# Performance work log

Hardware: AMD Instinct MI355X
Metric: run time of the kernel (lower is better)

## Reference

```python
import jax, jax.numpy as jnp
import numpy as np

POOLING_RATIO = 0.5  # matches init kwarg
N_NODES = 16384
N_EDGES = 524288
D_FEAT = 128


def setup_inputs() -> dict:
    key = jax.random.key(0)
    k1, k2, k3, k4 = jax.random.split(key, 4)
    return {
        "pos": jax.random.normal(k1, (N_NODES, 3), jnp.float32),
        "feat": jax.random.normal(k2, (N_NODES, D_FEAT), jnp.float32),
        "src": jax.random.randint(k3, (N_EDGES,), 0, N_NODES, jnp.int32),
        "dst": jax.random.randint(k4, (N_EDGES,), 0, N_NODES, jnp.int32),
        "batch_size": 4,
    }


def _fps(p, k):
    # Farthest point sampling on one cloud p: [n, 3]. Deterministic start at idx 0
    # (DGL uses a random start; we fix it for reproducibility).
    n = p.shape[0]
    def step(carry, _):
        dists, last = carry  # dists: min sq-dist to selected set so far
        d = jnp.sum((p - p[last]) ** 2, axis=-1)
        dists = jnp.minimum(dists, d)
        nxt = jnp.argmax(dists).astype(jnp.int32)
        return (dists, nxt), last
    init = (jnp.full((n,), 1e10, p.dtype), jnp.asarray(0, jnp.int32))
    _, idx = jax.lax.scan(step, init, None, length=k)
    return idx  # [k]


def reference(pos, feat, src, dst, batch_size):
    N = pos.shape[0]
    n_points = N // batch_size
    k = round(n_points * (1.0 - POOLING_RATIO))  # downsampled points per cloud

    # ---- farthest point sampling per cloud ----
    p = pos.reshape(batch_size, n_points, pos.shape[-1])  # [B, n, 3]
    fp = jax.vmap(lambda q: _fps(q, k))(p)                # [B, k] local ids
    offs = (jnp.arange(batch_size, dtype=jnp.int32) * n_points)[:, None]
    fp_idx = (fp + offs).reshape(-1)                      # [B*k] global ids

    # ---- copy_u + mean aggregation on the FULL graph (G.update_all) ----
    deg = jax.ops.segment_sum(jnp.ones_like(dst, dtype=feat.dtype), dst, num_segments=N)
    agg = jax.ops.segment_sum(feat[src], dst, num_segments=N)  # [N, D]
    agg = agg / jnp.maximum(deg, 1.0)[:, None]  # nodes with no in-edges stay 0

    # ---- induced subgraph gather ----
    M = fp_idx.shape[0]
    sub_x = pos[fp_idx]      # [M, 3]
    sub_feat = agg[fp_idx]   # [M, D]

    # induced subgraph edges: keep original edges whose endpoints are both sampled
    inv = jnp.full((N,), -1, jnp.int32).at[fp_idx].set(jnp.arange(M, dtype=jnp.int32))
    ls, ld = inv[src], inv[dst]
    edge_mask = (ls >= 0) & (ld >= 0)
    ls = jnp.where(edge_mask, ls, 0)
    ld = jnp.where(edge_mask, ld, 0)

    # per-edge displacement and norm on subgraph positions
    d = jnp.where(edge_mask[:, None], sub_x[ld] - sub_x[ls], 0.0)  # [E, 3]
    w = jnp.sqrt(jnp.sum(d ** 2, axis=-1, keepdims=True))          # [E, 1]

    return sub_x, sub_feat, d, w, edge_mask, fp_idx
```

## Files before the change

### kernel.cpp

```cpp
#include <hip/hip_runtime.h>
#include <math.h>

#define N_NODES 16384
#define N_EDGES 524288
#define D_FEAT  128
#define BATCH   4
#define NPTS    4096
#define KSEL    2048
#define MSEL    (BATCH*KSEL)


#define X16(F) F(0) F(1) F(2) F(3) F(4) F(5) F(6) F(7) \
               F(8) F(9) F(10) F(11) F(12) F(13) F(14) F(15)

__device__ __forceinline__ unsigned long long dpp_max_step(unsigned long long p,
                                                           unsigned int slo,
                                                           unsigned int shi)
{
    unsigned long long s = (((unsigned long long)shi) << 32) | slo;
    return (s > p) ? s : p;
}

__launch_bounds__(256, 1)
__global__ void fps_kernel(const float* __restrict__ pos,
                           int* __restrict__ fp_int,
                           int* __restrict__ inv,
                           float* __restrict__ out_subx,
                           float* __restrict__ out_fp)
{
    __shared__ float sx[NPTS];
    __shared__ float sy[NPTS];
    __shared__ float sz[NPTS];
    __shared__ int   sel[KSEL];
    __shared__ unsigned long long pwv[2][4];

    const int b   = blockIdx.x;
    const int tid = threadIdx.x;

    const float* gp = pos + (size_t)b * NPTS * 3;
    for (int i = tid; i < NPTS; i += 256) {
        sx[i] = gp[3 * i + 0];
        sy[i] = gp[3 * i + 1];
        sz[i] = gp[3 * i + 2];
    }
    __syncthreads();

#define DECL(J) float x##J, y##J, z##J, d##J;
    X16(DECL)
#undef DECL
#define LOAD(J) { int li = (J)*256 + tid; x##J = sx[li]; y##J = sy[li]; z##J = sz[li]; d##J = 1e10f; }
    X16(LOAD)
#undef LOAD

    int cur = 0;
    for (int t = 0; t < KSEL; ++t) {
        if (tid == 0) sel[t] = cur;
        float qx = sx[cur];
        float qy = sy[cur];
        float qz = sz[cur];

        float bv = -1.0f;
        int   bi = 0x7fffffff;
#define UPD(J) { \
        float dx = __fsub_rn(x##J, qx); \
        float dy = __fsub_rn(y##J, qy); \
        float dz = __fsub_rn(z##J, qz); \
        float dd = __fadd_rn(__fadd_rn(__fmul_rn(dx, dx), __fmul_rn(dy, dy)), \
                             __fmul_rn(dz, dz)); \
        d##J = fminf(d##J, dd); \
        if (d##J > bv) { bv = d##J; bi = (J)*256 + tid; } }
        X16(UPD)
#undef UPD

        unsigned long long p =
            (((unsigned long long)__float_as_uint(bv)) << 32) |
            (unsigned int)(~bi);

        {
            unsigned int lo, hi, slo, shi;
#define DSTEP(CTRL) \
            lo = (unsigned int)p; hi = (unsigned int)(p >> 32); \
            slo = __builtin_amdgcn_update_dpp(0, (int)lo, CTRL, 0xf, 0xf, true); \
            shi = __builtin_amdgcn_update_dpp(0, (int)hi, CTRL, 0xf, 0xf, true); \
            p = dpp_max_step(p, slo, shi);
            DSTEP(0x111)
            DSTEP(0x112)
            DSTEP(0x114)
            DSTEP(0x118)
            DSTEP(0x142)
            DSTEP(0x143)
#undef DSTEP
        }

        int par = t & 1;
        if ((tid & 63) == 63) pwv[par][tid >> 6] = p;
        __syncthreads();

        unsigned long long c0 = pwv[par][0];
        unsigned long long c1 = pwv[par][1];
        unsigned long long c2 = pwv[par][2];
        unsigned long long c3 = pwv[par][3];
        unsigned long long m01 = (c0 > c1) ? c0 : c1;
        unsigned long long m23 = (c2 > c3) ? c2 : c3;
        unsigned long long mm  = (m01 > m23) ? m01 : m23;
        cur = (int)(~(unsigned int)(mm & 0xffffffffULL));
    }
    __syncthreads();

    for (int t = tid; t < KSEL; t += 256) {
        int c = sel[t];
        int g = b * NPTS + c;
        int m = b * KSEL + t;
        fp_int[m] = g;
        inv[g] = m;
        out_fp[m] = (float)g;
        out_subx[m * 3 + 0] = sx[c];
        out_subx[m * 3 + 1] = sy[c];
        out_subx[m * 3 + 2] = sz[c];
    }
}

__global__ void deg_kernel(const int* __restrict__ dst, int* __restrict__ deg)
{
    int e = blockIdx.x * blockDim.x + threadIdx.x;
    if (e < N_EDGES) atomicAdd(&deg[dst[e]], 1);
}

__global__ void scan_kernel(const int* __restrict__ deg, int* __restrict__ row_ptr)
{
    __shared__ int part[1024];
    int tid = threadIdx.x;
    int base = tid * 16;
    int local[16];
    int s = 0;
#pragma unroll
    for (int j = 0; j < 16; ++j) { local[j] = s; s += deg[base + j]; }
    part[tid] = s;
    __syncthreads();
    for (int off = 1; off < 1024; off <<= 1) {
        int v = part[tid];
        int add = (tid >= off) ? part[tid - off] : 0;
        __syncthreads();
        part[tid] = v + add;
        __syncthreads();
    }
    int prefix = (tid == 0) ? 0 : part[tid - 1];
#pragma unroll
    for (int j = 0; j < 16; ++j) row_ptr[base + j] = prefix + local[j];
    if (tid == 1023) row_ptr[N_NODES] = part[1023];
}

__global__ void scatter_kernel(const int* __restrict__ src, const int* __restrict__ dst,
                               const int* __restrict__ row_ptr, int* __restrict__ cursor,
                               int* __restrict__ col)
{
    int e = blockIdx.x * blockDim.x + threadIdx.x;
    if (e < N_EDGES) {
        int d0 = dst[e];
        int r = atomicAdd(&cursor[d0], 1);
        col[row_ptr[d0] + r] = src[e];
    }
}

__global__ void agg_kernel(const float* __restrict__ feat,
                           const int* __restrict__ fp_int,
                           const int* __restrict__ row_ptr,
                           const int* __restrict__ col,
                           const int* __restrict__ deg,
                           float* __restrict__ out_subfeat)
{
    int wid  = (blockIdx.x * blockDim.x + threadIdx.x) >> 6;
    int lane = threadIdx.x & 63;
    if (wid >= MSEL) return;
    int v  = fp_int[wid];
    int s0 = row_ptr[v];
    int s1 = row_ptr[v + 1];
    float a0 = 0.0f, a1 = 0.0f;
    for (int e = s0; e < s1; ++e) {
        int s = col[e];
        const float2* f2 = (const float2*)(feat + (size_t)s * D_FEAT);
        float2 vv = f2[lane];
        a0 += vv.x;
        a1 += vv.y;
    }
    float dv = fmaxf((float)deg[v], 1.0f);
    float* o = out_subfeat + (size_t)wid * D_FEAT + lane * 2;
    o[0] = a0 / dv;
    o[1] = a1 / dv;
}

__global__ void edge_kernel(const int* __restrict__ src, const int* __restrict__ dst,
                            const int* __restrict__ inv, const float* __restrict__ subx,
                            float* __restrict__ outd, float* __restrict__ outw,
                            float* __restrict__ outm)
{
    int e = blockIdx.x * blockDim.x + threadIdx.x;
    if (e >= N_EDGES) return;
    int ls = inv[src[e]];
    int ld = inv[dst[e]];
    bool mk = (ls >= 0) && (ld >= 0);
    float dx = 0.0f, dy = 0.0f, dz = 0.0f;
    if (mk) {
        dx = __fsub_rn(subx[ld * 3 + 0], subx[ls * 3 + 0]);
        dy = __fsub_rn(subx[ld * 3 + 1], subx[ls * 3 + 1]);
        dz = __fsub_rn(subx[ld * 3 + 2], subx[ls * 3 + 2]);
    }
    float w = sqrtf(__fadd_rn(__fadd_rn(__fmul_rn(dx, dx), __fmul_rn(dy, dy)),
                              __fmul_rn(dz, dz)));
    outd[e * 3 + 0] = dx;
    outd[e * 3 + 1] = dy;
    outd[e * 3 + 2] = dz;
    outw[e] = w;
    outm[e] = mk ? 1.0f : 0.0f;
}

extern "C" void kernel_launch(void* const* d_in, const int* in_sizes, int n_in,
                              void* d_out, int out_size, void* d_ws, size_t ws_size,
                              hipStream_t stream)
{
    const float* pos  = (const float*)d_in[0];
    const float* feat = (const float*)d_in[1];
    const int*   src  = (const int*)d_in[2];
    const int*   dst  = (const int*)d_in[3];

    float* out = (float*)d_out;
    float* out_subx    = out;
    float* out_subfeat = out_subx + (size_t)MSEL * 3;
    float* out_d       = out_subfeat + (size_t)MSEL * D_FEAT;
    float* out_w       = out_d + (size_t)N_EDGES * 3;
    float* out_m       = out_w + (size_t)N_EDGES;
    float* out_fp      = out_m + (size_t)N_EDGES;

    int* fp_int  = (int*)d_ws;
    int* inv     = fp_int + MSEL;
    int* deg     = inv + N_NODES;
    int* row_ptr = deg + N_NODES;
    int* cursor  = row_ptr + (N_NODES+1);
    int* col     = cursor + N_NODES;

    hipMemsetAsync(inv,    0xFF, (size_t)N_NODES * 4, stream);
    hipMemsetAsync(deg,    0,    (size_t)N_NODES * 4, stream);
    hipMemsetAsync(cursor, 0,    (size_t)N_NODES * 4, stream);

    deg_kernel<<<N_EDGES / 256, 256, 0, stream>>>(dst, deg);
    scan_kernel<<<1, 1024, 0, stream>>>(deg, row_ptr);
    scatter_kernel<<<N_EDGES / 256, 256, 0, stream>>>(src, dst, row_ptr, cursor, col);

    fps_kernel<<<BATCH, 256, 0, stream>>>(pos, fp_int, inv, out_subx, out_fp);

    agg_kernel<<<(MSEL * 64) / 256, 256, 0, stream>>>(feat, fp_int, row_ptr, col, deg,
                                                      out_subfeat);
    edge_kernel<<<N_EDGES / 256, 256, 0, stream>>>(src, dst, inv, out_subx,
                                                   out_d, out_w, out_m);
}
```

Measured before the change: 1.273 ms.

## Split FPS argmax into float max then index DPP reductions; fuse agg and edge kernels

The per-iteration FPS argmax is restructured. A per-thread tree over the 16 register slots replaces the serial compare chain. The wavefront reduction now does a 32-bit float max via DPP, then a second 32-bit DPP max over inverted indices of matching lanes, instead of emulating 64-bit compares with paired DPP moves. This shortens the serial critical path of the 2048-step loop, which runs on only 4 blocks. The aggregation and edge kernels are also merged into one launch, which saves a launch and lets the two independent workloads overlap.

```diff
diff --git a/kernel.cpp b/kernel.cpp
--- a/kernel.cpp
+++ b/kernel.cpp
@@ -9,16 +9,20 @@
 #define KSEL    2048
 #define MSEL    (BATCH*KSEL)
 
-
 #define X16(F) F(0) F(1) F(2) F(3) F(4) F(5) F(6) F(7) \
                F(8) F(9) F(10) F(11) F(12) F(13) F(14) F(15)
 
-__device__ __forceinline__ unsigned long long dpp_max_step(unsigned long long p,
-                                                           unsigned int slo,
-                                                           unsigned int shi)
-{
-    unsigned long long s = (((unsigned long long)shi) << 32) | slo;
-    return (s > p) ? s : p;
+
+template <int CTRL>
+__device__ __forceinline__ float dpp_f32(float v)
+{
+    return __int_as_float(
+        __builtin_amdgcn_update_dpp(0, __float_as_int(v), CTRL, 0xf, 0xf, true));
+}
+template <int CTRL>
+__device__ __forceinline__ unsigned dpp_u32(unsigned v)
+{
+    return (unsigned)__builtin_amdgcn_update_dpp(0, (int)v, CTRL, 0xf, 0xf, true);
 }
 
 __launch_bounds__(256, 1)
@@ -34,8 +38,10 @@
     __shared__ int   sel[KSEL];
     __shared__ unsigned long long pwv[2][4];
 
-    const int b   = blockIdx.x;
-    const int tid = threadIdx.x;
+    const int b    = blockIdx.x;
+    const int tid  = threadIdx.x;
+    const int lane = tid & 63;
+    const int wv   = tid >> 6;
 
     const float* gp = pos + (size_t)b * NPTS * 3;
     for (int i = tid; i < NPTS; i += 256) {
@@ -59,41 +65,51 @@
         float qy = sy[cur];
         float qz = sz[cur];
 
-        float bv = -1.0f;
-        int   bi = 0x7fffffff;
 #define UPD(J) { \
         float dx = __fsub_rn(x##J, qx); \
         float dy = __fsub_rn(y##J, qy); \
         float dz = __fsub_rn(z##J, qz); \
         float dd = __fadd_rn(__fadd_rn(__fmul_rn(dx, dx), __fmul_rn(dy, dy)), \
                              __fmul_rn(dz, dz)); \
-        d##J = fminf(d##J, dd); \
-        if (d##J > bv) { bv = d##J; bi = (J)*256 + tid; } }
+        d##J = fminf(d##J, dd); }
         X16(UPD)
 #undef UPD
 
-        unsigned long long p =
-            (((unsigned long long)__float_as_uint(bv)) << 32) |
-            (unsigned int)(~bi);
-
-        {
-            unsigned int lo, hi, slo, shi;
-#define DSTEP(CTRL) \
-            lo = (unsigned int)p; hi = (unsigned int)(p >> 32); \
-            slo = __builtin_amdgcn_update_dpp(0, (int)lo, CTRL, 0xf, 0xf, true); \
-            shi = __builtin_amdgcn_update_dpp(0, (int)hi, CTRL, 0xf, 0xf, true); \
-            p = dpp_max_step(p, slo, shi);
-            DSTEP(0x111)
-            DSTEP(0x112)
-            DSTEP(0x114)
-            DSTEP(0x118)
-            DSTEP(0x142)
-            DSTEP(0x143)
-#undef DSTEP
-        }
+#define NODE(VA, JA, VB, JB, VO, JO) \
+        float VO = (VB > VA) ? VB : VA; int JO = (VB > VA) ? JB : JA;
+        NODE(d0,  0, d1,  1,  v01, j01)  NODE(d2,  2, d3,  3,  v23, j23)
+        NODE(d4,  4, d5,  5,  v45, j45)  NODE(d6,  6, d7,  7,  v67, j67)
+        NODE(d8,  8, d9,  9,  v89, j89)  NODE(d10,10, d11,11,  vab, jab)
+        NODE(d12,12, d13,13,  vcd, jcd)  NODE(d14,14, d15,15,  vef, jef)
+        NODE(v01, j01, v23, j23, vA, jA) NODE(v45, j45, v67, j67, vB, jB)
+        NODE(v89, j89, vab, jab, vC, jC) NODE(vcd, jcd, vef, jef, vD, jD)
+        NODE(vA, jA, vB, jB, vE, jE)     NODE(vC, jC, vD, jD, vF, jF)
+        NODE(vE, jE, vF, jF, bv, bj)
+#undef NODE
+        int bi = bj * 256 + tid;
+
+        float rv = bv;
+        rv = fmaxf(rv, dpp_f32<0x111>(rv));
+        rv = fmaxf(rv, dpp_f32<0x112>(rv));
+        rv = fmaxf(rv, dpp_f32<0x114>(rv));
+        rv = fmaxf(rv, dpp_f32<0x118>(rv));
+        rv = fmaxf(rv, dpp_f32<0x142>(rv));
+        rv = fmaxf(rv, dpp_f32<0x143>(rv));
+        unsigned smax_u = (unsigned)__builtin_amdgcn_readlane(__float_as_int(rv), 63);
+
+        unsigned cand = (__float_as_uint(bv) == smax_u) ? ~(unsigned)bi : 0u;
+        cand = max(cand, dpp_u32<0x111>(cand));
+        cand = max(cand, dpp_u32<0x112>(cand));
+        cand = max(cand, dpp_u32<0x114>(cand));
+        cand = max(cand, dpp_u32<0x118>(cand));
+        cand = max(cand, dpp_u32<0x142>(cand));
+        cand = max(cand, dpp_u32<0x143>(cand));
+        unsigned winv = (unsigned)__builtin_amdgcn_readlane((int)cand, 63);
+
+        unsigned long long p = (((unsigned long long)smax_u) << 32) | winv;
 
         int par = t & 1;
-        if ((tid & 63) == 63) pwv[par][tid >> 6] = p;
+        if (lane == 0) pwv[par][wv] = p;
         __syncthreads();
 
         unsigned long long c0 = pwv[par][0];
@@ -103,7 +119,7 @@
         unsigned long long m01 = (c0 > c1) ? c0 : c1;
         unsigned long long m23 = (c2 > c3) ? c2 : c3;
         unsigned long long mm  = (m01 > m23) ? m01 : m23;
-        cur = (int)(~(unsigned int)(mm & 0xffffffffULL));
+        cur = (int)(~(unsigned)(mm & 0xffffffffULL));
     }
     __syncthreads();
 
@@ -162,56 +178,57 @@
     }
 }
 
-__global__ void agg_kernel(const float* __restrict__ feat,
-                           const int* __restrict__ fp_int,
-                           const int* __restrict__ row_ptr,
-                           const int* __restrict__ col,
-                           const int* __restrict__ deg,
-                           float* __restrict__ out_subfeat)
-{
-    int wid  = (blockIdx.x * blockDim.x + threadIdx.x) >> 6;
-    int lane = threadIdx.x & 63;
-    if (wid >= MSEL) return;
-    int v  = fp_int[wid];
-    int s0 = row_ptr[v];
-    int s1 = row_ptr[v + 1];
-    float a0 = 0.0f, a1 = 0.0f;
-    for (int e = s0; e < s1; ++e) {
-        int s = col[e];
-        const float2* f2 = (const float2*)(feat + (size_t)s * D_FEAT);
-        float2 vv = f2[lane];
-        a0 += vv.x;
-        a1 += vv.y;
-    }
-    float dv = fmaxf((float)deg[v], 1.0f);
-    float* o = out_subfeat + (size_t)wid * D_FEAT + lane * 2;
-    o[0] = a0 / dv;
-    o[1] = a1 / dv;
-}
-
-__global__ void edge_kernel(const int* __restrict__ src, const int* __restrict__ dst,
-                            const int* __restrict__ inv, const float* __restrict__ subx,
-                            float* __restrict__ outd, float* __restrict__ outw,
-                            float* __restrict__ outm)
-{
-    int e = blockIdx.x * blockDim.x + threadIdx.x;
-    if (e >= N_EDGES) return;
-    int ls = inv[src[e]];
-    int ld = inv[dst[e]];
-    bool mk = (ls >= 0) && (ld >= 0);
-    float dx = 0.0f, dy = 0.0f, dz = 0.0f;
-    if (mk) {
-        dx = __fsub_rn(subx[ld * 3 + 0], subx[ls * 3 + 0]);
-        dy = __fsub_rn(subx[ld * 3 + 1], subx[ls * 3 + 1]);
-        dz = __fsub_rn(subx[ld * 3 + 2], subx[ls * 3 + 2]);
-    }
-    float w = sqrtf(__fadd_rn(__fadd_rn(__fmul_rn(dx, dx), __fmul_rn(dy, dy)),
-                              __fmul_rn(dz, dz)));
-    outd[e * 3 + 0] = dx;
-    outd[e * 3 + 1] = dy;
-    outd[e * 3 + 2] = dz;
-    outw[e] = w;
-    outm[e] = mk ? 1.0f : 0.0f;
+__global__ void agg_edge_kernel(const float* __restrict__ feat,
+                                const int* __restrict__ fp_int,
+                                const int* __restrict__ row_ptr,
+                                const int* __restrict__ col,
+                                const int* __restrict__ deg,
+                                float* __restrict__ out_subfeat,
+                                const int* __restrict__ src,
+                                const int* __restrict__ dst,
+                                const int* __restrict__ inv,
+                                const float* __restrict__ subx,
+                                float* __restrict__ outd,
+                                float* __restrict__ outw,
+                                float* __restrict__ outm)
+{
+    if (blockIdx.x < 2048) {
+        int wid  = (blockIdx.x * blockDim.x + threadIdx.x) >> 6;
+        int lane = threadIdx.x & 63;
+        int v  = fp_int[wid];
+        int s0 = row_ptr[v];
+        int s1 = row_ptr[v + 1];
+        float a0 = 0.0f, a1 = 0.0f;
+        for (int e = s0; e < s1; ++e) {
+            int s = col[e];
+            const float2* f2 = (const float2*)(feat + (size_t)s * D_FEAT);
+            float2 vv = f2[lane];
+            a0 += vv.x;
+            a1 += vv.y;
+        }
+        float dv = fmaxf((float)deg[v], 1.0f);
+        float* o = out_subfeat + (size_t)wid * D_FEAT + lane * 2;
+        o[0] = a0 / dv;
+        o[1] = a1 / dv;
+    } else {
+        int e = (blockIdx.x - 2048) * blockDim.x + threadIdx.x;
+        int ls = inv[src[e]];
+        int ld = inv[dst[e]];
+        bool mk = (ls >= 0) && (ld >= 0);
+        float dx = 0.0f, dy = 0.0f, dz = 0.0f;
+        if (mk) {
+            dx = __fsub_rn(subx[ld * 3 + 0], subx[ls * 3 + 0]);
+            dy = __fsub_rn(subx[ld * 3 + 1], subx[ls * 3 + 1]);
+            dz = __fsub_rn(subx[ld * 3 + 2], subx[ls * 3 + 2]);
+        }
+        float w = sqrtf(__fadd_rn(__fadd_rn(__fmul_rn(dx, dx), __fmul_rn(dy, dy)),
+                                  __fmul_rn(dz, dz)));
+        outd[e * 3 + 0] = dx;
+        outd[e * 3 + 1] = dy;
+        outd[e * 3 + 2] = dz;
+        outw[e] = w;
+        outm[e] = mk ? 1.0f : 0.0f;
+    }
 }
 
 extern "C" void kernel_launch(void* const* d_in, const int* in_sizes, int n_in,
@@ -238,9 +255,9 @@
     int* cursor  = row_ptr + (N_NODES+1);
     int* col     = cursor + N_NODES;
 
-    hipMemsetAsync(inv,    0xFF, (size_t)N_NODES * 4, stream);
-    hipMemsetAsync(deg,    0,    (size_t)N_NODES * 4, stream);
-    hipMemsetAsync(cursor, 0,    (size_t)N_NODES * 4, stream);
+    (void)hipMemsetAsync(inv,    0xFF, (size_t)N_NODES * 4, stream);
+    (void)hipMemsetAsync(deg,    0,    (size_t)N_NODES * 4, stream);
+    (void)hipMemsetAsync(cursor, 0,    (size_t)N_NODES * 4, stream);
 
     deg_kernel<<<N_EDGES / 256, 256, 0, stream>>>(dst, deg);
     scan_kernel<<<1, 1024, 0, stream>>>(deg, row_ptr);
@@ -248,8 +265,7 @@
 
     fps_kernel<<<BATCH, 256, 0, stream>>>(pos, fp_int, inv, out_subx, out_fp);
 
-    agg_kernel<<<(MSEL * 64) / 256, 256, 0, stream>>>(feat, fp_int, row_ptr, col, deg,
-                                                      out_subfeat);
-    edge_kernel<<<N_EDGES / 256, 256, 0, stream>>>(src, dst, inv, out_subx,
-                                                   out_d, out_w, out_m);
-}
+    agg_edge_kernel<<<4096, 256, 0, stream>>>(feat, fp_int, row_ptr, col, deg,
+                                              out_subfeat, src, dst, inv, out_subx,
+                                              out_d, out_w, out_m);
+}
```

New measurement: 1.419 ms. 11.5% more time.
